# Kernel optimization log

Measured on AMD Instinct MI355X. Metric: run time of the kernel, lower is better.

## Reference

```python
import math
import jax, jax.numpy as jnp
import numpy as np

N_STEPS = 5
STEP = 0.1      # step_size buffer (eval mode: never updated)
LMBD = 0.1
MU = 0.0
N_DICT = 1


def _prox(c):
    # elasnet_prox: softshrink(c * s_mu, lmbd*step * s_mu); with mu=0, s_mu=1
    s_mu = 1.0 / (1.0 + MU * STEP)
    lam = LMBD * STEP * s_mu
    c = c * s_mu
    return jnp.sign(c) * jnp.maximum(jnp.abs(c) - lam, 0.0)


def _fista(x, W):
    # x: [N, C], W: [D, C]; F.linear(x, W) == x @ W.T
    s = STEP
    # i == 0
    c = jax.nn.relu(_prox(s * (x @ W.T)))
    # i == 1
    c_pre = c
    r = x - c @ W                      # residual [N, C]
    c = jax.nn.relu(_prox(c + s * (r @ W.T)))
    t = (math.sqrt(5.0) + 1.0) / 2.0
    # i >= 2: FISTA momentum, gradient evaluated at c (as in source)
    for _ in range(2, N_STEPS):
        t_pre = t
        t = (math.sqrt(1.0 + 4.0 * t_pre * t_pre) + 1.0) / 2.0
        a = (t_pre + t - 1.0) / t * c + (1.0 - t_pre) / t * c_pre
        c_pre = c
        r = x - c @ W
        c = jax.nn.relu(_prox(a + s * (r @ W.T)))
    return c


def setup_inputs() -> dict:
    key = jax.random.key(0)
    k1, k2 = jax.random.split(key)
    x = jax.random.normal(k1, (8, 2048, 512), dtype=jnp.float32)
    # kaiming-uniform-like dictionary [dict_size, n_channel]
    bound = math.sqrt(6.0 / 512.0)
    weight = jax.random.uniform(k2, (2048, 512), dtype=jnp.float32,
                                minval=-bound, maxval=bound)
    return {"x": x, "weight": weight}


def reference(x, weight):
    bs, tok, dim = x.shape
    xf = x.reshape(-1, dim)                    # [N, C]
    c = _fista(xf, weight)                     # [N, D]
    xp = c @ weight                            # [N, C]
    r = xf - xp
    r_loss = jnp.sum(r * r) / N_DICT
    c_loss = LMBD * jnp.sum(jnp.abs(c)) + 0.5 * MU * jnp.sum(c * c)
    return (c.reshape(bs, tok, -1), xp.reshape(bs, tok, -1), r, r_loss, c_loss)
```

## Files before the change

kernel.cpp:

```cpp
#include <hip/hip_runtime.h>
#include <cmath>


typedef __attribute__((ext_vector_type(8))) short bf16x8;
typedef __attribute__((ext_vector_type(8))) unsigned short u16x8;
typedef __attribute__((ext_vector_type(4))) float f32x4;

constexpr float S_STEP = 0.1f;
constexpr float LAM    = 0.01f;

__device__ __forceinline__ unsigned short f2bf(float f) {
    unsigned u = __float_as_uint(f);
    u += 0x7FFFu + ((u >> 16) & 1u);
    return (unsigned short)(u >> 16);
}
__device__ __forceinline__ float bf2f(unsigned short s) {
    return __uint_as_float(((unsigned)s) << 16);
}

__device__ __forceinline__ void async16(const void* g, void* l) {
    __builtin_amdgcn_global_load_lds(
        (const __attribute__((address_space(1))) void*)g,
        (__attribute__((address_space(3))) void*)l, 16, 0, 0);
}

template<int EPI>
__global__ __launch_bounds__(256)
void gemm_bt(const short* __restrict__ A, const short* __restrict__ B,
             int K, int Nn, int lbx,
             const unsigned short* Cc, const unsigned short* Cpre,
             const unsigned short* __restrict__ Xb, const float* __restrict__ Xf,
             unsigned short* OutB, float* Out32, float* R32,
             float cfA, float cfB, float* loss)
{
    __shared__ __align__(16) unsigned char smem[49152];
    short* S  = (short*)smem;
    float (*L)[132] = (float (*)[132])smem;
    float* red2 = (float*)(smem + 49088);

    const int tid  = threadIdx.x;
    const int wave = tid >> 6;
    const int lane = tid & 63;

    const int qchunk = gridDim.x >> 3;
    const int idx    = (blockIdx.x & 7) * qchunk + (blockIdx.x >> 3);
    const int rowBase = (idx >> lbx) * 128;
    const int colBase = (idx & ((1 << lbx) - 1)) * 128;

    const int sRow = lane >> 2;
    const int sK   = (lane & 3) << 3;
    const short* gA = A + (size_t)(rowBase + wave * 32 + sRow) * K + sK;
    const short* gB = B + (size_t)(colBase + wave * 32 + sRow) * K + sK;
    const size_t rstep = (size_t)16 * K;
    short* lA = S + wave * 1024;
    short* lB = S + 4096 + wave * 1024;

    const int m16  = lane & 15;
    const int quad = lane >> 4;
    const short* paBase = S + ((wave & 1) * 64 + m16) * 32 + quad * 8;
    const short* pbBase = S + 4096 + ((wave >> 1) * 64 + m16) * 32 + quad * 8;

    f32x4 acc[4][4] = {};
    const int nIter = K >> 5;

    {
        async16(gA,         lA);
        async16(gA + rstep, lA + 512);
        async16(gB,         lB);
        async16(gB + rstep, lB + 512);
        if (nIter > 1) {
            async16(gA + 32,         lA + 8192);
            async16(gA + 32 + rstep, lA + 8192 + 512);
            async16(gB + 32,         lB + 8192);
            async16(gB + 32 + rstep, lB + 8192 + 512);
            asm volatile("s_waitcnt vmcnt(4)" ::: "memory");
        } else {
            asm volatile("s_waitcnt vmcnt(0)" ::: "memory");
        }
        __builtin_amdgcn_s_barrier();
    }

    int sSt = 2;
    int sRd = 0;
    for (int it = 0; it < nIter; ++it) {
        if (it + 2 < nIter) {
            const int kb = (it + 2) << 5;
            short* sA = lA + sSt * 8192;
            short* sB = lB + sSt * 8192;
            async16(gA + kb,         sA);
            async16(gA + kb + rstep, sA + 512);
            async16(gB + kb,         sB);
            async16(gB + kb + rstep, sB + 512);
        }
        const int cb = sRd * 8192;
        bf16x8 af[4], bfr[4];
        #pragma unroll
        for (int i = 0; i < 4; ++i) af[i]  = *(const bf16x8*)(paBase + cb + i * 512);
        #pragma unroll
        for (int j = 0; j < 4; ++j) bfr[j] = *(const bf16x8*)(pbBase + cb + j * 512);
        #pragma unroll
        for (int i = 0; i < 4; ++i)
            #pragma unroll
            for (int j = 0; j < 4; ++j)
                acc[i][j] = __builtin_amdgcn_mfma_f32_16x16x32_bf16(
                                af[i], bfr[j], acc[i][j], 0, 0, 0);
        if (it + 2 < nIter)      asm volatile("s_waitcnt vmcnt(4)" ::: "memory");
        else if (it + 1 < nIter) asm volatile("s_waitcnt vmcnt(0)" ::: "memory");
        if (it + 1 < nIter) __builtin_amdgcn_s_barrier();
        sSt = (sSt == 2) ? 0 : sSt + 1;
        sRd = (sRd == 2) ? 0 : sRd + 1;
    }

    const int lrow = tid >> 3;
    const int seg  = tid & 7;
    const bool useCp = (cfB != 0.f);
    float lsum = 0.f;

    auto gofs = [&](int t) -> size_t {
        return (size_t)(rowBase + t * 32 + lrow) * Nn + colBase + seg * 16;
    };

    u16x8 cc0{}, cc1{}, cp0{}, cp1{}, xq0{}, xq1{};
    float xfv[16];
    if constexpr (EPI == 1 || EPI == 2) {
        const size_t g = gofs(0);
        cc0 = *(const u16x8*)(Cc + g); cc1 = *(const u16x8*)(Cc + g + 8);
        if (useCp) { cp0 = *(const u16x8*)(Cpre + g); cp1 = *(const u16x8*)(Cpre + g + 8); }
    } else if constexpr (EPI == 3) {
        const size_t g = gofs(0);
        xq0 = *(const u16x8*)(Xb + g); xq1 = *(const u16x8*)(Xb + g + 8);
    } else if constexpr (EPI == 4) {
        const size_t g = gofs(0);
        #pragma unroll
        for (int q = 0; q < 4; ++q)
            *(f32x4*)&xfv[q * 4] = *(const f32x4*)(Xf + g + q * 4);
    }

    #pragma unroll
    for (int t = 0; t < 4; ++t) {
        __syncthreads();
        if ((wave & 1) == (t >> 1)) {
            #pragma unroll
            for (int ii = 0; ii < 2; ++ii) {
                const int i   = (t & 1) * 2 + ii;
                const int lr0 = ii * 16 + quad * 4;
                #pragma unroll
                for (int r = 0; r < 4; ++r)
                    #pragma unroll
                    for (int j = 0; j < 4; ++j)
                        L[lr0 + r][(wave >> 1) * 64 + j * 16 + m16] = acc[i][j][r];
            }
        }
        __syncthreads();

        float v[16];
        #pragma unroll
        for (int q = 0; q < 4; ++q)
            *(f32x4*)&v[q * 4] = *(const f32x4*)&L[lrow][seg * 16 + q * 4];

        const size_t gidx = gofs(t);

        u16x8 ncc0{}, ncc1{}, ncp0{}, ncp1{}, nxq0{}, nxq1{};
        float nxfv[16];
        if (t < 3) {
            const size_t gn = gofs(t + 1);
            if constexpr (EPI == 1 || EPI == 2) {
                ncc0 = *(const u16x8*)(Cc + gn); ncc1 = *(const u16x8*)(Cc + gn + 8);
                if (useCp) { ncp0 = *(const u16x8*)(Cpre + gn); ncp1 = *(const u16x8*)(Cpre + gn + 8); }
            } else if constexpr (EPI == 3) {
                nxq0 = *(const u16x8*)(Xb + gn); nxq1 = *(const u16x8*)(Xb + gn + 8);
            } else if constexpr (EPI == 4) {
                #pragma unroll
                for (int q = 0; q < 4; ++q)
                    *(f32x4*)&nxfv[q * 4] = *(const f32x4*)(Xf + gn + q * 4);
            }
        }

        if constexpr (EPI == 0) {
            u16x8 o0, o1;
            #pragma unroll
            for (int k = 0; k < 8; ++k) {
                o0[k] = f2bf(fmaxf(S_STEP * v[k]     - LAM, 0.f));
                o1[k] = f2bf(fmaxf(S_STEP * v[k + 8] - LAM, 0.f));
            }
            *(u16x8*)(OutB + gidx)     = o0;
            *(u16x8*)(OutB + gidx + 8) = o1;
        } else if constexpr (EPI == 1 || EPI == 2) {
            float w[16];
            #pragma unroll
            for (int k = 0; k < 8; ++k) {
                w[k]     = fmaxf(cfA * bf2f(cc0[k]) + cfB * bf2f(cp0[k])
                                 + S_STEP * v[k]     - LAM, 0.f);
                w[k + 8] = fmaxf(cfA * bf2f(cc1[k]) + cfB * bf2f(cp1[k])
                                 + S_STEP * v[k + 8] - LAM, 0.f);
            }
            u16x8 o0, o1;
            #pragma unroll
            for (int k = 0; k < 8; ++k) { o0[k] = f2bf(w[k]); o1[k] = f2bf(w[k + 8]); }
            *(u16x8*)(OutB + gidx)     = o0;
            *(u16x8*)(OutB + gidx + 8) = o1;
            if constexpr (EPI == 2) {
                #pragma unroll
                for (int q = 0; q < 4; ++q)
                    *(f32x4*)(Out32 + gidx + q * 4) = *(const f32x4*)&w[q * 4];
                #pragma unroll
                for (int k = 0; k < 16; ++k) lsum += w[k];
            }
        } else if constexpr (EPI == 3) {
            u16x8 o0, o1;
            #pragma unroll
            for (int k = 0; k < 8; ++k) {
                o0[k] = f2bf(bf2f(xq0[k]) - v[k]);
                o1[k] = f2bf(bf2f(xq1[k]) - v[k + 8]);
            }
            *(u16x8*)(OutB + gidx)     = o0;
            *(u16x8*)(OutB + gidx + 8) = o1;
        } else {
            float rv[16];
            #pragma unroll
            for (int k = 0; k < 16; ++k) {
                rv[k] = xfv[k] - v[k];
                lsum += rv[k] * rv[k];
            }
            #pragma unroll
            for (int q = 0; q < 4; ++q) {
                *(f32x4*)(Out32 + gidx + q * 4) = *(const f32x4*)&v[q * 4];
                *(f32x4*)(R32   + gidx + q * 4) = *(const f32x4*)&rv[q * 4];
            }
        }

        if (t < 3) {
            if constexpr (EPI == 1 || EPI == 2) {
                cc0 = ncc0; cc1 = ncc1;
                if (useCp) { cp0 = ncp0; cp1 = ncp1; }
            } else if constexpr (EPI == 3) {
                xq0 = nxq0; xq1 = nxq1;
            } else if constexpr (EPI == 4) {
                #pragma unroll
                for (int k = 0; k < 16; ++k) xfv[k] = nxfv[k];
            }
        }
    }

    if constexpr (EPI == 2 || EPI == 4) {
        #pragma unroll
        for (int off = 32; off; off >>= 1) lsum += __shfl_down(lsum, off, 64);
        if (lane == 0) red2[wave] = lsum;
        __syncthreads();
        if (tid == 0) {
            const float s = red2[0] + red2[1] + red2[2] + red2[3];
            atomicAdd(loss, (EPI == 2) ? 0.1f * s : s);
        }
    }
}

__global__ __launch_bounds__(256)
void cvt_w_k(const float* __restrict__ W,
             unsigned short* __restrict__ Wb, unsigned short* __restrict__ Wtb)
{
    __shared__ unsigned short T[64][65];
    const int dBase = blockIdx.y * 64;
    const int cBase = blockIdx.x * 64;
    const int lc = threadIdx.x & 63;
    const int lr = threadIdx.x >> 6;
    #pragma unroll
    for (int p = 0; p < 16; ++p) {
        const int dl = p * 4 + lr;
        const size_t idx = (size_t)(dBase + dl) * 512 + cBase + lc;
        const unsigned short b = f2bf(W[idx]);
        Wb[idx] = b;
        T[dl][lc] = b;
    }
    __syncthreads();
    #pragma unroll
    for (int p = 0; p < 16; ++p) {
        const int cl = p * 4 + lr;
        Wtb[(size_t)(cBase + cl) * 2048 + dBase + lc] = T[lc][cl];
    }
}

__global__ __launch_bounds__(256)
void cvt_x_k(const float4* __restrict__ x4, ushort4* __restrict__ xb4, int n4)
{
    for (int i = blockIdx.x * 256 + threadIdx.x; i < n4; i += gridDim.x * 256) {
        const float4 v = x4[i];
        xb4[i] = make_ushort4(f2bf(v.x), f2bf(v.y), f2bf(v.z), f2bf(v.w));
    }
}

__global__ __launch_bounds__(256)
void copy_wtb_k(const u16x8* __restrict__ src, u16x8* __restrict__ dst)
{
    const int i = blockIdx.x * 256 + threadIdx.x;
    dst[i] = src[i];
}

extern "C" void kernel_launch(void* const* d_in, const int* in_sizes, int n_in,
                              void* d_out, int out_size, void* d_ws, size_t ws_size,
                              hipStream_t stream)
{
    (void)in_sizes; (void)n_in; (void)out_size; (void)ws_size;

    constexpr int N = 16384, C = 512, D = 2048;
    constexpr size_t ND = (size_t)N * D;
    constexpr size_t NC = (size_t)N * C;

    const float* x = (const float*)d_in[0];
    const float* W = (const float*)d_in[1];

    float* out    = (float*)d_out;
    float* c_out  = out;
    float* xp_out = out + ND;
    float* r_out  = out + ND + NC;
    float* rloss  = out + ND + 2 * NC;
    float* closs  = rloss + 1;

    short* cb0 = (short*)d_ws;
    short* cb1 = cb0 + ND;

    unsigned short* rb  = (unsigned short*)xp_out;
    unsigned short* Wb  = (unsigned short*)xp_out + NC;
    unsigned short* Wtb = (unsigned short*)r_out;
    unsigned short* xb  = (unsigned short*)r_out + (size_t)D * C;

    hipMemsetAsync((void*)rloss, 0, 2 * sizeof(float), stream);

    double tp = (std::sqrt(5.0) + 1.0) / 2.0;
    float cfA[5] = {0.f, 1.f, 0.f, 0.f, 0.f};
    float cfB[5] = {0.f, 0.f, 0.f, 0.f, 0.f};
    for (int i = 2; i < 5; ++i) {
        double t = (std::sqrt(1.0 + 4.0 * tp * tp) + 1.0) / 2.0;
        cfA[i] = (float)((tp + t - 1.0) / t);
        cfB[i] = (float)((1.0 - tp) / t);
        tp = t;
    }

    const dim3 blk(256);
    cvt_w_k<<<dim3(C / 64, D / 64), blk, 0, stream>>>(W, Wb, Wtb);
    cvt_x_k<<<dim3(1024), blk, 0, stream>>>((const float4*)x, (ushort4*)xb,
                                            (int)(NC / 4));

    const dim3 gridD((D / 128) * (N / 128));
    const dim3 gridC((C / 128) * (N / 128));
    constexpr int LBX_D = 4, LBX_C = 2;

    gemm_bt<0><<<gridD, blk, 0, stream>>>((const short*)xb, (const short*)Wb,
                                          C, D, LBX_D, nullptr, nullptr,
                                          nullptr, nullptr,
                                          (unsigned short*)cb0, nullptr, nullptr,
                                          0.f, 0.f, nullptr);

    short* bufs[2] = {cb0, cb1};
    for (int i = 1; i < 5; ++i) {
        const short* cprev = bufs[(i - 1) & 1];
        short*       cnew  = bufs[i & 1];
        const unsigned short* cpre2 =
            (i == 1) ? (const unsigned short*)cprev : (const unsigned short*)cnew;
        gemm_bt<3><<<gridC, blk, 0, stream>>>(cprev, (const short*)Wtb,
                                              D, C, LBX_C, nullptr, nullptr,
                                              xb, nullptr,
                                              rb, nullptr, nullptr,
                                              0.f, 0.f, nullptr);
        if (i < 4)
            gemm_bt<1><<<gridD, blk, 0, stream>>>((const short*)rb, (const short*)Wb,
                                                  C, D, LBX_D,
                                                  (const unsigned short*)cprev,
                                                  cpre2, nullptr, nullptr,
                                                  (unsigned short*)cnew, nullptr,
                                                  nullptr, cfA[i], cfB[i], nullptr);
        else
            gemm_bt<2><<<gridD, blk, 0, stream>>>((const short*)rb, (const short*)Wb,
                                                  C, D, LBX_D,
                                                  (const unsigned short*)cprev,
                                                  cpre2, nullptr, nullptr,
                                                  (unsigned short*)cnew, c_out,
                                                  nullptr, cfA[i], cfB[i], closs);
    }

    copy_wtb_k<<<dim3(512), blk, 0, stream>>>((const u16x8*)Wtb, (u16x8*)cb1);

    gemm_bt<4><<<gridC, blk, 0, stream>>>(cb0, (const short*)cb1,
                                          D, C, LBX_C, nullptr, nullptr,
                                          nullptr, x,
                                          nullptr, xp_out, r_out,
                                          0.f, 0.f, rloss);
}
```

Before: 718.3 us.

## Use 256x128 tiles with 512-thread blocks for the dictionary-width GEMMs

Adds a specialized gemm_bt256 kernel with 512 threads (8 waves) computing 256x128 output tiles with K fixed at 512, and uses it for the xW^T and rW^T GEMMs producing the 2048-wide code matrix. Each B tile is now shared across twice as many rows, which halves the number of blocks and reduces redundant B loads from global memory. The generic kernel loses its EPI 0/1/2 paths and the unused parameters. The larger LDS footprint (72KB) and 512-thread blocks may limit occupancy.

```diff
diff --git a/kernel.cpp b/kernel.cpp
--- a/kernel.cpp
+++ b/kernel.cpp
@@ -25,13 +25,185 @@
 }
 
 template<int EPI>
+__global__ __launch_bounds__(512, 4)
+void gemm_bt256(const short* __restrict__ A, const short* __restrict__ B,
+                const unsigned short* __restrict__ Cc,
+                const unsigned short* __restrict__ Cpre,
+                unsigned short* __restrict__ OutB, float* __restrict__ Out32,
+                float cfA, float cfB, float* __restrict__ loss)
+{
+    constexpr int K = 512, Nn = 2048, NT = 16;
+    __shared__ __align__(16) unsigned char smem[73728];
+    short* S  = (short*)smem;
+    float (*L)[132] = (float (*)[132])smem;
+    float* red2 = (float*)(smem + 73696);
+
+    const int tid  = threadIdx.x;
+    const int wave = tid >> 6;
+    const int lane = tid & 63;
+    const int wr   = wave >> 1;
+    const int wc   = wave & 1;
+    const int m16  = lane & 15;
+    const int quad = lane >> 4;
+
+    const int idx = (blockIdx.x & 7) * 128 + (blockIdx.x >> 3);
+    const int rowBase = (idx >> 4) * 256;
+    const int colBase = (idx & 15) * 128;
+
+    const int sRow = lane >> 2;
+    const int sK   = (lane & 3) << 3;
+    const short* gA0 = A + (size_t)(rowBase + wave * 32 + sRow) * K + sK;
+    const short* gB0 = B + (size_t)(colBase + wave * 16 + sRow) * K + sK;
+    const size_t rstep16 = (size_t)16 * K;
+    short* lA = S + wave * 1024;
+    short* lB = S + 8192 + wave * 512;
+
+    const short* paBase = S + (wr * 64 + m16) * 32 + quad * 8;
+    const short* pbBase = S + 8192 + (wc * 64 + m16) * 32 + quad * 8;
+
+    f32x4 acc[4][4] = {};
+
+    {
+        async16(gA0,           lA);
+        async16(gA0 + rstep16, lA + 512);
+        async16(gB0,           lB);
+        async16(gA0 + 32,           lA + 12288);
+        async16(gA0 + 32 + rstep16, lA + 12288 + 512);
+        async16(gB0 + 32,           lB + 12288);
+        asm volatile("s_waitcnt vmcnt(3)" ::: "memory");
+        __builtin_amdgcn_s_barrier();
+    }
+
+    int sSt = 2, sRd = 0;
+    for (int it = 0; it < NT; ++it) {
+        if (it + 2 < NT) {
+            const int kb = (it + 2) << 5;
+            short* sA = lA + sSt * 12288;
+            short* sB = lB + sSt * 12288;
+            async16(gA0 + kb,           sA);
+            async16(gA0 + kb + rstep16, sA + 512);
+            async16(gB0 + kb,           sB);
+        }
+        const int cb = sRd * 12288;
+        bf16x8 af[4], bfr[4];
+        #pragma unroll
+        for (int i = 0; i < 4; ++i) af[i]  = *(const bf16x8*)(paBase + cb + i * 512);
+        #pragma unroll
+        for (int j = 0; j < 4; ++j) bfr[j] = *(const bf16x8*)(pbBase + cb + j * 512);
+        #pragma unroll
+        for (int i = 0; i < 4; ++i)
+            #pragma unroll
+            for (int j = 0; j < 4; ++j)
+                acc[i][j] = __builtin_amdgcn_mfma_f32_16x16x32_bf16(
+                                af[i], bfr[j], acc[i][j], 0, 0, 0);
+        if (it + 2 < NT)      asm volatile("s_waitcnt vmcnt(3)" ::: "memory");
+        else if (it + 1 < NT) asm volatile("s_waitcnt vmcnt(0)" ::: "memory");
+        if (it + 1 < NT) __builtin_amdgcn_s_barrier();
+        sSt = (sSt == 2) ? 0 : sSt + 1;
+        sRd = (sRd == 2) ? 0 : sRd + 1;
+    }
+
+    const int lrow = tid >> 4;
+    const int seg  = tid & 15;
+    const bool useCp = (cfB != 0.f);
+    float lsum = 0.f;
+
+    auto gofs = [&](int t) -> size_t {
+        return (size_t)(rowBase + t * 32 + lrow) * Nn + colBase + seg * 8;
+    };
+
+    u16x8 cc{}, cp{};
+    if constexpr (EPI == 1 || EPI == 2) {
+        const size_t g = gofs(0);
+        cc = *(const u16x8*)(Cc + g);
+        if (useCp) cp = *(const u16x8*)(Cpre + g);
+    }
+
+    #pragma unroll
+    for (int t = 0; t < 8; ++t) {
+        __syncthreads();
+        if (wr == (t >> 1)) {
+            #pragma unroll
+            for (int ii = 0; ii < 2; ++ii) {
+                const int i   = (t & 1) * 2 + ii;
+                const int lr0 = ii * 16 + quad * 4;
+                #pragma unroll
+                for (int r = 0; r < 4; ++r)
+                    #pragma unroll
+                    for (int j = 0; j < 4; ++j)
+                        L[lr0 + r][wc * 64 + j * 16 + m16] = acc[i][j][r];
+            }
+        }
+        __syncthreads();
+
+        float v[8];
+        *(f32x4*)&v[0] = *(const f32x4*)&L[lrow][seg * 8];
+        *(f32x4*)&v[4] = *(const f32x4*)&L[lrow][seg * 8 + 4];
+
+        const size_t gidx = gofs(t);
+
+        u16x8 ncc{}, ncp{};
+        if (t < 7) {
+            if constexpr (EPI == 1 || EPI == 2) {
+                const size_t gn = gofs(t + 1);
+                ncc = *(const u16x8*)(Cc + gn);
+                if (useCp) ncp = *(const u16x8*)(Cpre + gn);
+            }
+        }
+
+        if constexpr (EPI == 0) {
+            u16x8 o;
+            #pragma unroll
+            for (int k = 0; k < 8; ++k)
+                o[k] = f2bf(fmaxf(S_STEP * v[k] - LAM, 0.f));
+            *(u16x8*)(OutB + gidx) = o;
+        } else {
+            float w[8];
+            u16x8 o;
+            #pragma unroll
+            for (int k = 0; k < 8; ++k) {
+                w[k] = fmaxf(cfA * bf2f(cc[k]) + cfB * bf2f(cp[k])
+                             + S_STEP * v[k] - LAM, 0.f);
+                o[k] = f2bf(w[k]);
+            }
+            *(u16x8*)(OutB + gidx) = o;
+            if constexpr (EPI == 2) {
+                *(f32x4*)(Out32 + gidx)     = *(const f32x4*)&w[0];
+                *(f32x4*)(Out32 + gidx + 4) = *(const f32x4*)&w[4];
+                #pragma unroll
+                for (int k = 0; k < 8; ++k) lsum += w[k];
+            }
+        }
+
+        if (t < 7) {
+            if constexpr (EPI == 1 || EPI == 2) {
+                cc = ncc;
+                if (useCp) cp = ncp;
+            }
+        }
+    }
+
+    if constexpr (EPI == 2) {
+        #pragma unroll
+        for (int off = 32; off; off >>= 1) lsum += __shfl_down(lsum, off, 64);
+        if (lane == 0) red2[wave] = lsum;
+        __syncthreads();
+        if (tid == 0) {
+            float s = 0.f;
+            #pragma unroll
+            for (int wv = 0; wv < 8; ++wv) s += red2[wv];
+            atomicAdd(loss, 0.1f * s);
+        }
+    }
+}
+
+template<int EPI>
 __global__ __launch_bounds__(256)
 void gemm_bt(const short* __restrict__ A, const short* __restrict__ B,
              int K, int Nn, int lbx,
-             const unsigned short* Cc, const unsigned short* Cpre,
              const unsigned short* __restrict__ Xb, const float* __restrict__ Xf,
-             unsigned short* OutB, float* Out32, float* R32,
-             float cfA, float cfB, float* loss)
+             unsigned short* __restrict__ OutB, float* Out32, float* R32,
+             float* loss)
 {
     __shared__ __align__(16) unsigned char smem[49152];
     short* S  = (short*)smem;
@@ -68,20 +240,15 @@
         async16(gA + rstep, lA + 512);
         async16(gB,         lB);
         async16(gB + rstep, lB + 512);
-        if (nIter > 1) {
-            async16(gA + 32,         lA + 8192);
-            async16(gA + 32 + rstep, lA + 8192 + 512);
-            async16(gB + 32,         lB + 8192);
-            async16(gB + 32 + rstep, lB + 8192 + 512);
-            asm volatile("s_waitcnt vmcnt(4)" ::: "memory");
-        } else {
-            asm volatile("s_waitcnt vmcnt(0)" ::: "memory");
-        }
+        async16(gA + 32,         lA + 8192);
+        async16(gA + 32 + rstep, lA + 8192 + 512);
+        async16(gB + 32,         lB + 8192);
+        async16(gB + 32 + rstep, lB + 8192 + 512);
+        asm volatile("s_waitcnt vmcnt(4)" ::: "memory");
         __builtin_amdgcn_s_barrier();
     }
 
-    int sSt = 2;
-    int sRd = 0;
+    int sSt = 2, sRd = 0;
     for (int it = 0; it < nIter; ++it) {
         if (it + 2 < nIter) {
             const int kb = (it + 2) << 5;
@@ -113,20 +280,15 @@
 
     const int lrow = tid >> 3;
     const int seg  = tid & 7;
-    const bool useCp = (cfB != 0.f);
     float lsum = 0.f;
 
     auto gofs = [&](int t) -> size_t {
         return (size_t)(rowBase + t * 32 + lrow) * Nn + colBase + seg * 16;
     };
 
-    u16x8 cc0{}, cc1{}, cp0{}, cp1{}, xq0{}, xq1{};
+    u16x8 xq0{}, xq1{};
     float xfv[16];
-    if constexpr (EPI == 1 || EPI == 2) {
-        const size_t g = gofs(0);
-        cc0 = *(const u16x8*)(Cc + g); cc1 = *(const u16x8*)(Cc + g + 8);
-        if (useCp) { cp0 = *(const u16x8*)(Cpre + g); cp1 = *(const u16x8*)(Cpre + g + 8); }
-    } else if constexpr (EPI == 3) {
+    if constexpr (EPI == 3) {
         const size_t g = gofs(0);
         xq0 = *(const u16x8*)(Xb + g); xq1 = *(const u16x8*)(Xb + g + 8);
     } else if constexpr (EPI == 4) {
@@ -160,14 +322,11 @@
 
         const size_t gidx = gofs(t);
 
-        u16x8 ncc0{}, ncc1{}, ncp0{}, ncp1{}, nxq0{}, nxq1{};
+        u16x8 nxq0{}, nxq1{};
         float nxfv[16];
         if (t < 3) {
             const size_t gn = gofs(t + 1);
-            if constexpr (EPI == 1 || EPI == 2) {
-                ncc0 = *(const u16x8*)(Cc + gn); ncc1 = *(const u16x8*)(Cc + gn + 8);
-                if (useCp) { ncp0 = *(const u16x8*)(Cpre + gn); ncp1 = *(const u16x8*)(Cpre + gn + 8); }
-            } else if constexpr (EPI == 3) {
+            if constexpr (EPI == 3) {
                 nxq0 = *(const u16x8*)(Xb + gn); nxq1 = *(const u16x8*)(Xb + gn + 8);
             } else if constexpr (EPI == 4) {
                 #pragma unroll
@@ -176,37 +335,7 @@
             }
         }
 
-        if constexpr (EPI == 0) {
-            u16x8 o0, o1;
-            #pragma unroll
-            for (int k = 0; k < 8; ++k) {
-                o0[k] = f2bf(fmaxf(S_STEP * v[k]     - LAM, 0.f));
-                o1[k] = f2bf(fmaxf(S_STEP * v[k + 8] - LAM, 0.f));
-            }
-            *(u16x8*)(OutB + gidx)     = o0;
-            *(u16x8*)(OutB + gidx + 8) = o1;
-        } else if constexpr (EPI == 1 || EPI == 2) {
-            float w[16];
-            #pragma unroll
-            for (int k = 0; k < 8; ++k) {
-                w[k]     = fmaxf(cfA * bf2f(cc0[k]) + cfB * bf2f(cp0[k])
-                                 + S_STEP * v[k]     - LAM, 0.f);
-                w[k + 8] = fmaxf(cfA * bf2f(cc1[k]) + cfB * bf2f(cp1[k])
-                                 + S_STEP * v[k + 8] - LAM, 0.f);
-            }
-            u16x8 o0, o1;
-            #pragma unroll
-            for (int k = 0; k < 8; ++k) { o0[k] = f2bf(w[k]); o1[k] = f2bf(w[k + 8]); }
-            *(u16x8*)(OutB + gidx)     = o0;
-            *(u16x8*)(OutB + gidx + 8) = o1;
-            if constexpr (EPI == 2) {
-                #pragma unroll
-                for (int q = 0; q < 4; ++q)
-                    *(f32x4*)(Out32 + gidx + q * 4) = *(const f32x4*)&w[q * 4];
-                #pragma unroll
-                for (int k = 0; k < 16; ++k) lsum += w[k];
-            }
-        } else if constexpr (EPI == 3) {
+        if constexpr (EPI == 3) {
             u16x8 o0, o1;
             #pragma unroll
             for (int k = 0; k < 8; ++k) {
@@ -230,10 +359,7 @@
         }
 
         if (t < 3) {
-            if constexpr (EPI == 1 || EPI == 2) {
-                cc0 = ncc0; cc1 = ncc1;
-                if (useCp) { cp0 = ncp0; cp1 = ncp1; }
-            } else if constexpr (EPI == 3) {
+            if constexpr (EPI == 3) {
                 xq0 = nxq0; xq1 = nxq1;
             } else if constexpr (EPI == 4) {
                 #pragma unroll
@@ -242,15 +368,13 @@
         }
     }
 
-    if constexpr (EPI == 2 || EPI == 4) {
+    if constexpr (EPI == 4) {
         #pragma unroll
         for (int off = 32; off; off >>= 1) lsum += __shfl_down(lsum, off, 64);
         if (lane == 0) red2[wave] = lsum;
         __syncthreads();
-        if (tid == 0) {
-            const float s = red2[0] + red2[1] + red2[2] + red2[3];
-            atomicAdd(loss, (EPI == 2) ? 0.1f * s : s);
-        }
+        if (tid == 0)
+            atomicAdd(loss, red2[0] + red2[1] + red2[2] + red2[3]);
     }
 }
 
@@ -336,19 +460,18 @@
     }
 
     const dim3 blk(256);
+    const dim3 blk512(512);
     cvt_w_k<<<dim3(C / 64, D / 64), blk, 0, stream>>>(W, Wb, Wtb);
     cvt_x_k<<<dim3(1024), blk, 0, stream>>>((const float4*)x, (ushort4*)xb,
                                             (int)(NC / 4));
 
-    const dim3 gridD((D / 128) * (N / 128));
+    const dim3 gridD((N / 256) * (D / 128));
     const dim3 gridC((C / 128) * (N / 128));
-    constexpr int LBX_D = 4, LBX_C = 2;
-
-    gemm_bt<0><<<gridD, blk, 0, stream>>>((const short*)xb, (const short*)Wb,
-                                          C, D, LBX_D, nullptr, nullptr,
-                                          nullptr, nullptr,
-                                          (unsigned short*)cb0, nullptr, nullptr,
-                                          0.f, 0.f, nullptr);
+    constexpr int LBX_C = 2;
+
+    gemm_bt256<0><<<gridD, blk512, 0, stream>>>(
+        (const short*)xb, (const short*)Wb, nullptr, nullptr,
+        (unsigned short*)cb0, nullptr, 0.f, 0.f, nullptr);
 
     short* bufs[2] = {cb0, cb1};
     for (int i = 1; i < 5; ++i) {
@@ -357,31 +480,25 @@
         const unsigned short* cpre2 =
             (i == 1) ? (const unsigned short*)cprev : (const unsigned short*)cnew;
         gemm_bt<3><<<gridC, blk, 0, stream>>>(cprev, (const short*)Wtb,
-                                              D, C, LBX_C, nullptr, nullptr,
+                                              D, C, LBX_C,
                                               xb, nullptr,
-                                              rb, nullptr, nullptr,
-                                              0.f, 0.f, nullptr);
+                                              rb, nullptr, nullptr, nullptr);
         if (i < 4)
-            gemm_bt<1><<<gridD, blk, 0, stream>>>((const short*)rb, (const short*)Wb,
-                                                  C, D, LBX_D,
-                                                  (const unsigned short*)cprev,
-                                                  cpre2, nullptr, nullptr,
-                                                  (unsigned short*)cnew, nullptr,
-                                                  nullptr, cfA[i], cfB[i], nullptr);
+            gemm_bt256<1><<<gridD, blk512, 0, stream>>>(
+                (const short*)rb, (const short*)Wb,
+                (const unsigned short*)cprev, cpre2,
+                (unsigned short*)cnew, nullptr, cfA[i], cfB[i], nullptr);
         else
-            gemm_bt<2><<<gridD, blk, 0, stream>>>((const short*)rb, (const short*)Wb,
-                                                  C, D, LBX_D,
-                                                  (const unsigned short*)cprev,
-                                                  cpre2, nullptr, nullptr,
-                                                  (unsigned short*)cnew, c_out,
-                                                  nullptr, cfA[i], cfB[i], closs);
+            gemm_bt256<2><<<gridD, blk512, 0, stream>>>(
+                (const short*)rb, (const short*)Wb,
+                (const unsigned short*)cprev, cpre2,
+                (unsigned short*)cnew, c_out, cfA[i], cfB[i], closs);
     }
 
     copy_wtb_k<<<dim3(512), blk, 0, stream>>>((const u16x8*)Wtb, (u16x8*)cb1);
 
     gemm_bt<4><<<gridC, blk, 0, stream>>>(cb0, (const short*)cb1,
-                                          D, C, LBX_C, nullptr, nullptr,
+                                          D, C, LBX_C,
                                           nullptr, x,
-                                          nullptr, xp_out, r_out,
-                                          0.f, 0.f, rloss);
-}
+                                          nullptr, xp_out, r_out, rloss);
+}
```

Result: no change. 731.4 us (+1.8%).
